# Kernel tuning notes

Measured on AMD Instinct MI355X. Metric: run time of the kernel, lower is better.

Reference implementation:

```python
import jax, jax.numpy as jnp
import numpy as np

H = 1024
E = 8
TOP_K = 2
B, S = 4, 2048


def setup_inputs() -> dict:
    key = jax.random.key(0)
    ks = jax.random.split(key, 8)
    scale = 0.02
    return {
        "x": jax.random.normal(ks[0], (B, S, H), dtype=jnp.float32),
        "router_w": jax.random.normal(ks[1], (H, E), dtype=jnp.float32) * scale,
        "router_b": jnp.zeros((E,), dtype=jnp.float32),
        "w1": jax.random.normal(ks[2], (E, H, 4 * H), dtype=jnp.float32) * scale,
        "b1": jnp.zeros((E, 4 * H), dtype=jnp.float32),
        "w2": jax.random.normal(ks[3], (E, 4 * H, H), dtype=jnp.float32) * scale,
        "b2": jnp.zeros((E, H), dtype=jnp.float32),
    }


def reference(x, router_w, router_b, w1, b1, w2, b2):
    b, s, h = x.shape
    n_exp = w1.shape[0]
    x_flat = x.reshape(-1, h)  # [T, H]
    T = x_flat.shape[0]

    # Router: softmax then top-k, renormalize top-k probs (matches torch code).
    logits = x_flat @ router_w + router_b            # [T, E]
    probs = jax.nn.softmax(logits, axis=-1)
    top_values, top_indices = jax.lax.top_k(probs, TOP_K)  # [T, k]
    top_values = top_values / jnp.sum(top_values, axis=-1, keepdims=True)

    # Per-token combine weight for each expert (0 if token not routed there).
    combine = jnp.zeros((T, n_exp), dtype=x.dtype)
    combine = combine.at[jnp.arange(T)[:, None], top_indices].add(top_values)  # [T, E]

    # Loop over the small fixed expert set; masked combine weights zero out
    # contributions from unrouted tokens, matching the gather/scatter original.
    out = jnp.zeros_like(x_flat)
    for e in range(n_exp):
        hmid = jax.nn.gelu(x_flat @ w1[e] + b1[e], approximate=False)  # [T, 4H]
        y = hmid @ w2[e] + b2[e]                                       # [T, H]
        out = out + combine[:, e:e + 1] * y
    return out.reshape(b, s, h)
```

## Files before the change

kernel.cpp:

```cpp
#include <hip/hip_runtime.h>
#include <hip/hip_bf16.h>
#include <math.h>

#define TT 8192
#define HD 1024
#define FHD 4096
#define NE 8
#define NTMAX 136
#define NWG1 4352

typedef short s16x8 __attribute__((ext_vector_type(8)));
typedef float f32x4 __attribute__((ext_vector_type(4)));
using bf16 = __hip_bfloat16;
typedef unsigned int u32;

#define OFF_COUNTS 0
#define OFF_DONE   32
#define OFF_CURSOR 64
#define OFF_OFFS   128
#define OFF_E0     256
#define OFF_E1     (OFF_E0 + 4*TT)
#define OFF_W0     (OFF_E1 + 4*TT)
#define OFF_W1     (OFF_W0 + 4*TT)
#define OFF_S0     (OFF_W1 + 4*TT)
#define OFF_S1     (OFF_S0 + 4*TT)
#define OFF_TID    (OFF_S1 + 4*TT)
#define OFF_TW     (OFF_TID + 8*TT)
#define OFF_TMR    (OFF_TW + 8*TT)
#define OFF_TME    (OFF_TMR + 4*144)
#define OFF_TMN    (OFF_TME + 4*144)
#define OFF_XBF    (OFF_TMN + 64)
#define OFF_W1T    (OFF_XBF + 2*TT*HD)
#define OFF_W2T    (OFF_W1T + 2*NE*HD*FHD)
#define OFF_HMID   (OFF_W2T + 2*NE*HD*FHD)
#define OFF_YS     (OFF_HMID + (size_t)2*(2*TT)*FHD)

__device__ __forceinline__ void gload_lds16(const void* g, void* l) {
    __builtin_amdgcn_global_load_lds(
        (const __attribute__((address_space(1))) u32*)g,
        (__attribute__((address_space(3))) u32*)l, 16, 0, 0);
}

__device__ __forceinline__ void transpose_panel(const float* __restrict__ in,
        bf16* __restrict__ out, int R, int C, int rem, int tid, char* smem) {
    float (*tile)[65]  = reinterpret_cast<float(*)[65]>(smem);
    bf16  (*btile)[264] = reinterpret_cast<bf16(*)[264]>(smem + 16640);
    int kch = R >> 8, nch = C >> 6;
    int per = kch * nch;
    int e = rem / per;
    int rem2 = rem % per;
    int kc = rem2 / nch, nc = rem2 % nch;
    int k0 = kc << 8, n0 = nc << 6;
    const float* ine = in + (size_t)e * R * C;
    bf16* oute = out + (size_t)e * R * C;
    for (int s = 0; s < 4; ++s) {
        int ks = k0 + s * 64;
#pragma unroll
        for (int i = 0; i < 4; ++i) {
            int lin = tid + i * 256;
            int r = lin >> 4, cg = lin & 15;
            float4 v = *reinterpret_cast<const float4*>(&ine[(size_t)(ks + r) * C + n0 + cg * 4]);
            tile[r][cg * 4 + 0] = v.x; tile[r][cg * 4 + 1] = v.y;
            tile[r][cg * 4 + 2] = v.z; tile[r][cg * 4 + 3] = v.w;
        }
        __syncthreads();
#pragma unroll
        for (int i = 0; i < 4; ++i) {
            int lin = tid + i * 256;
            int n = lin >> 4, kg = lin & 15;
            bf16 h[4];
            h[0] = __float2bfloat16(tile[kg * 4 + 0][n]);
            h[1] = __float2bfloat16(tile[kg * 4 + 1][n]);
            h[2] = __float2bfloat16(tile[kg * 4 + 2][n]);
            h[3] = __float2bfloat16(tile[kg * 4 + 3][n]);
            *reinterpret_cast<uint2*>(&btile[n][s * 64 + kg * 4]) = *reinterpret_cast<uint2*>(h);
        }
        __syncthreads();
    }
#pragma unroll
    for (int i = 0; i < 8; ++i) {
        int lin = tid + i * 256;
        int n = lin >> 5, kk = lin & 31;
        *reinterpret_cast<uint4*>(&oute[(size_t)(n0 + n) * R + k0 + kk * 8]) =
            *reinterpret_cast<const uint4*>(&btile[n][kk * 8]);
    }
}

__global__ __launch_bounds__(256) void fused1_kernel(
        const float* __restrict__ x, const float* __restrict__ rw, const float* __restrict__ rb,
        const float* __restrict__ w1, bf16* __restrict__ xbf, bf16* __restrict__ w1t,
        int* __restrict__ e0a, int* __restrict__ e1a,
        float* __restrict__ w0a, float* __restrict__ w1a,
        int* __restrict__ counts, int* __restrict__ done,
        int* __restrict__ offs, int* __restrict__ cursor,
        int* __restrict__ tmr, int* __restrict__ tme, int* __restrict__ tmn) {
    __shared__ __attribute__((aligned(16))) char smem[50432];
    int bid = blockIdx.x;
    int tid = threadIdx.x;
    if (bid < 2048) {
        transpose_panel(w1, w1t, HD, FHD, bid, tid, smem);
        return;
    }
    int rbid = bid - 2048;
    int wid = tid >> 6, lane = tid & 63;
    int t = rbid * 4 + wid;
    const float* xp = x + (size_t)t * HD + lane * 16;
    float xv[16];
#pragma unroll
    for (int j = 0; j < 4; ++j) {
        float4 v = *reinterpret_cast<const float4*>(&xp[j * 4]);
        xv[4 * j] = v.x; xv[4 * j + 1] = v.y; xv[4 * j + 2] = v.z; xv[4 * j + 3] = v.w;
    }
    {
        bf16 hv[16];
#pragma unroll
        for (int j = 0; j < 16; ++j) hv[j] = __float2bfloat16(xv[j]);
        uint4* dst = reinterpret_cast<uint4*>(&xbf[(size_t)t * HD + lane * 16]);
        dst[0] = reinterpret_cast<uint4*>(hv)[0];
        dst[1] = reinterpret_cast<uint4*>(hv)[1];
    }
    float acc[8] = {0.f, 0.f, 0.f, 0.f, 0.f, 0.f, 0.f, 0.f};
    const float* rp = rw + (size_t)(lane * 16) * NE;
#pragma unroll
    for (int hh = 0; hh < 16; ++hh) {
        float4 r0 = *reinterpret_cast<const float4*>(&rp[hh * 8]);
        float4 r1 = *reinterpret_cast<const float4*>(&rp[hh * 8 + 4]);
        acc[0] += xv[hh] * r0.x; acc[1] += xv[hh] * r0.y;
        acc[2] += xv[hh] * r0.z; acc[3] += xv[hh] * r0.w;
        acc[4] += xv[hh] * r1.x; acc[5] += xv[hh] * r1.y;
        acc[6] += xv[hh] * r1.z; acc[7] += xv[hh] * r1.w;
    }
#pragma unroll
    for (int e = 0; e < 8; ++e) {
#pragma unroll
        for (int off = 32; off > 0; off >>= 1) acc[e] += __shfl_xor(acc[e], off, 64);
    }
    if (lane == 0) {
        float lg[8];
#pragma unroll
        for (int e = 0; e < 8; ++e) lg[e] = acc[e] + rb[e];
        int a = 0;
#pragma unroll
        for (int e = 1; e < 8; ++e) if (lg[e] > lg[a]) a = e;
        int b = (a == 0) ? 1 : 0;
#pragma unroll
        for (int e = 0; e < 8; ++e) if (e != a && e != b && lg[e] > lg[b]) b = e;
        float wa = 1.0f / (1.0f + expf(lg[b] - lg[a]));
        float wb = 1.0f / (1.0f + expf(lg[a] - lg[b]));
        e0a[t] = a; e1a[t] = b; w0a[t] = wa; w1a[t] = wb;
        atomicAdd(&counts[a], 1);
        atomicAdd(&counts[b], 1);
    }
    __syncthreads();
    __shared__ int lastFlag;
    if (tid == 0) {
        __threadfence();
        lastFlag = (atomicAdd(done, 1) == 2047) ? 1 : 0;
    }
    __syncthreads();
    if (!lastFlag) return;
    __threadfence();
    __shared__ int cbase[NE + 1], tbase[NE + 1];
    if (tid == 0) {
        int s = 0, ntt = 0;
        for (int e = 0; e < NE; ++e) {
            int c = atomicAdd(&counts[e], 0);
            cbase[e] = s; tbase[e] = ntt;
            s += c; ntt += (c + 127) >> 7;
        }
        cbase[NE] = s; tbase[NE] = ntt;
        tmn[0] = ntt;
        offs[NE] = s;
    }
    __syncthreads();
    if (tid < NE) { offs[tid] = cbase[tid]; cursor[tid] = cbase[tid]; }
    if (tid < NTMAX) {
        int ntt = tbase[NE];
        if (tid < ntt) {
            int e = 0;
            while (tbase[e + 1] <= tid) ++e;
            tmr[tid] = cbase[e] + ((tid - tbase[e]) << 7);
            tme[tid] = e;
        } else { tmr[tid] = 0; tme[tid] = 0; }
    }
}

__global__ __launch_bounds__(256) void scatter_kernel(const int* __restrict__ e0a, const int* __restrict__ e1a,
        const float* __restrict__ w0a, const float* __restrict__ w1a,
        int* __restrict__ cursor, int* __restrict__ tid_arr, float* __restrict__ tw_arr,
        int* __restrict__ slot0, int* __restrict__ slot1) {
    int t = blockIdx.x * 256 + threadIdx.x;
    int s0 = atomicAdd(&cursor[e0a[t]], 1);
    tid_arr[s0] = t; tw_arr[s0] = w0a[t]; slot0[t] = s0;
    int s1 = atomicAdd(&cursor[e1a[t]], 1);
    tid_arr[s1] = t; tw_arr[s1] = w1a[t]; slot1[t] = s1;
}

__global__ __launch_bounds__(256) void fused2_kernel(
        const float* __restrict__ w2, bf16* __restrict__ w2t,
        const bf16* __restrict__ xbf, const bf16* __restrict__ w1t,
        const float* __restrict__ b1, const int* __restrict__ offs,
        const int* __restrict__ tid_arr, bf16* __restrict__ hmid,
        const int* __restrict__ tmr, const int* __restrict__ tme, const int* __restrict__ tmn) {
    __shared__ __attribute__((aligned(16))) char smem[50432];
    int bid = blockIdx.x;
    int tid = threadIdx.x;
    if (bid < 2048) {
        transpose_panel(w2, w2t, FHD, HD, bid, tid, smem);
        return;
    }
    bf16* As = reinterpret_cast<bf16*>(smem);
    bf16* Bs = reinterpret_cast<bf16*>(smem + 8192);
    int*  toks = reinterpret_cast<int*>(smem + 16384);
    int orig = bid - 2048;
    int wg = (orig & 7) * (NWG1 >> 3) + (orig >> 3);
    int st = wg / 68, within = wg % 68;
    int tidx = (st >> 3) * 17 + (within % 17);
    int nt = (st & 7) * 4 + (within / 17);
    if (tidx >= tmn[0]) return;
    int e = tme[tidx];
    int row0 = tmr[tidx];
    int s1 = offs[e + 1];
    int n0 = nt * 128;
    if (tid < 128) { int s = row0 + tid; toks[tid] = tid_arr[(s < s1) ? s : (s1 - 1)]; }
    __syncthreads();
    int lane = tid & 63, w = tid >> 6;
    int wrow = (w >> 1) * 64, wcol = (w & 1) * 64;
    int lr = lane & 15, lk = (lane >> 4) * 8;
    int srow = lane >> 2, seg = lane & 3;
    int tokA0 = toks[w * 32 + srow];
    int tokA1 = toks[w * 32 + 16 + srow];
    const bf16* w1e = w1t + (size_t)e * FHD * HD;
    const bf16* bsrc0 = w1e + (size_t)(n0 + w * 32 + srow) * HD + seg * 8;
    const bf16* bsrc1 = w1e + (size_t)(n0 + w * 32 + 16 + srow) * HD + seg * 8;
    const bf16* asrc0 = xbf + (size_t)tokA0 * HD + seg * 8;
    const bf16* asrc1 = xbf + (size_t)tokA1 * HD + seg * 8;
    bf16* aDst0 = &As[(w * 32) * 32];
    bf16* aDst1 = &As[(w * 32 + 16) * 32];
    bf16* bDst0 = &Bs[(w * 32) * 32];
    bf16* bDst1 = &Bs[(w * 32 + 16) * 32];
    f32x4 acc[4][4] = {};
    for (int k0 = 0; k0 < HD; k0 += 32) {
        gload_lds16(asrc0 + k0, aDst0);
        gload_lds16(asrc1 + k0, aDst1);
        gload_lds16(bsrc0 + k0, bDst0);
        gload_lds16(bsrc1 + k0, bDst1);
        __syncthreads();
        s16x8 aF[4], bF[4];
#pragma unroll
        for (int m = 0; m < 4; ++m) aF[m] = *reinterpret_cast<const s16x8*>(&As[(wrow + m * 16 + lr) * 32 + lk]);
#pragma unroll
        for (int n = 0; n < 4; ++n) bF[n] = *reinterpret_cast<const s16x8*>(&Bs[(wcol + n * 16 + lr) * 32 + lk]);
#pragma unroll
        for (int m = 0; m < 4; ++m)
#pragma unroll
            for (int n = 0; n < 4; ++n)
                acc[m][n] = __builtin_amdgcn_mfma_f32_16x16x32_bf16(aF[m], bF[n], acc[m][n], 0, 0, 0);
        __syncthreads();
    }
#pragma unroll
    for (int m = 0; m < 4; ++m) {
#pragma unroll
        for (int n = 0; n < 4; ++n) {
            int col = n0 + wcol + n * 16 + lr;
            float bv = b1[(size_t)e * FHD + col];
#pragma unroll
            for (int r = 0; r < 4; ++r) {
                int row = wrow + m * 16 + (lane >> 4) * 4 + r;
                int slot = row0 + row;
                if (slot < s1) {
                    float v2 = acc[m][n][r] + bv;
                    v2 = 0.5f * v2 * (1.0f + erff(v2 * 0.70710678118f));
                    hmid[(size_t)slot * FHD + col] = __float2bfloat16(v2);
                }
            }
        }
    }
}

__global__ __launch_bounds__(256) void gemm2_kernel(const bf16* __restrict__ hmid, const bf16* __restrict__ w2t,
        const float* __restrict__ b2, const int* __restrict__ offs, float* __restrict__ ys,
        const int* __restrict__ tmr, const int* __restrict__ tme, const int* __restrict__ tmn) {
    __shared__ bf16 As[128 * 32];
    __shared__ bf16 Bs[128 * 32];
    int nwg = gridDim.x;
    int orig = blockIdx.x;
    int wg = (orig & 7) * (nwg >> 3) + (orig >> 3);
    int st = wg / 34, within = wg % 34;
    int tidx = (st >> 2) * 17 + (within % 17);
    int nt = (st & 3) * 2 + (within / 17);
    if (tidx >= tmn[0]) return;
    int e = tme[tidx];
    int row0 = tmr[tidx];
    int s1 = offs[e + 1];
    int n0 = nt * 128;
    int tid = threadIdx.x;
    int lane = tid & 63, w = tid >> 6;
    int wrow = (w >> 1) * 64, wcol = (w & 1) * 64;
    int lr = lane & 15, lk = (lane >> 4) * 8;
    int srow = lane >> 2, seg = lane & 3;
    int ar0 = row0 + w * 32 + srow;      if (ar0 >= s1) ar0 = s1 - 1;
    int ar1 = row0 + w * 32 + 16 + srow; if (ar1 >= s1) ar1 = s1 - 1;
    const bf16* w2e = w2t + (size_t)e * HD * FHD;
    const bf16* bsrc0 = w2e + (size_t)(n0 + w * 32 + srow) * FHD + seg * 8;
    const bf16* bsrc1 = w2e + (size_t)(n0 + w * 32 + 16 + srow) * FHD + seg * 8;
    const bf16* asrc0 = hmid + (size_t)ar0 * FHD + seg * 8;
    const bf16* asrc1 = hmid + (size_t)ar1 * FHD + seg * 8;
    bf16* aDst0 = &As[(w * 32) * 32];
    bf16* aDst1 = &As[(w * 32 + 16) * 32];
    bf16* bDst0 = &Bs[(w * 32) * 32];
    bf16* bDst1 = &Bs[(w * 32 + 16) * 32];
    f32x4 acc[4][4] = {};
    for (int k0 = 0; k0 < FHD; k0 += 32) {
        gload_lds16(asrc0 + k0, aDst0);
        gload_lds16(asrc1 + k0, aDst1);
        gload_lds16(bsrc0 + k0, bDst0);
        gload_lds16(bsrc1 + k0, bDst1);
        __syncthreads();
        s16x8 aF[4], bF[4];
#pragma unroll
        for (int m = 0; m < 4; ++m) aF[m] = *reinterpret_cast<const s16x8*>(&As[(wrow + m * 16 + lr) * 32 + lk]);
#pragma unroll
        for (int n = 0; n < 4; ++n) bF[n] = *reinterpret_cast<const s16x8*>(&Bs[(wcol + n * 16 + lr) * 32 + lk]);
#pragma unroll
        for (int m = 0; m < 4; ++m)
#pragma unroll
            for (int n = 0; n < 4; ++n)
                acc[m][n] = __builtin_amdgcn_mfma_f32_16x16x32_bf16(aF[m], bF[n], acc[m][n], 0, 0, 0);
        __syncthreads();
    }
#pragma unroll
    for (int m = 0; m < 4; ++m) {
#pragma unroll
        for (int n = 0; n < 4; ++n) {
            int col = n0 + wcol + n * 16 + lr;
            float bv = b2[(size_t)e * HD + col];
#pragma unroll
            for (int r = 0; r < 4; ++r) {
                int row = wrow + m * 16 + (lane >> 4) * 4 + r;
                int slot = row0 + row;
                if (slot < s1) ys[(size_t)slot * HD + col] = acc[m][n][r] + bv;
            }
        }
    }
}

__global__ __launch_bounds__(256) void combine_kernel(const float* __restrict__ ys,
        const int* __restrict__ slot0, const int* __restrict__ slot1,
        const float* __restrict__ tw, float* __restrict__ out) {
    int t = blockIdx.x;
    int c = threadIdx.x * 4;
    int sa = slot0[t], sb = slot1[t];
    float wa = tw[sa], wb = tw[sb];
    float4 a = *reinterpret_cast<const float4*>(&ys[(size_t)sa * HD + c]);
    float4 b = *reinterpret_cast<const float4*>(&ys[(size_t)sb * HD + c]);
    float4 o;
    o.x = wa * a.x + wb * b.x; o.y = wa * a.y + wb * b.y;
    o.z = wa * a.z + wb * b.z; o.w = wa * a.w + wb * b.w;
    *reinterpret_cast<float4*>(&out[(size_t)t * HD + c]) = o;
}

extern "C" void kernel_launch(void* const* d_in, const int* in_sizes, int n_in,
                              void* d_out, int out_size, void* d_ws, size_t ws_size,
                              hipStream_t stream) {
    const float* x  = (const float*)d_in[0];
    const float* rw = (const float*)d_in[1];
    const float* rb = (const float*)d_in[2];
    const float* w1 = (const float*)d_in[3];
    const float* b1 = (const float*)d_in[4];
    const float* w2 = (const float*)d_in[5];
    const float* b2 = (const float*)d_in[6];
    float* out = (float*)d_out;
    char* ws = (char*)d_ws;

    int*   counts  = (int*)(ws + OFF_COUNTS);
    int*   done    = (int*)(ws + OFF_DONE);
    int*   cursor  = (int*)(ws + OFF_CURSOR);
    int*   offs    = (int*)(ws + OFF_OFFS);
    int*   e0a     = (int*)(ws + OFF_E0);
    int*   e1a     = (int*)(ws + OFF_E1);
    float* w0a     = (float*)(ws + OFF_W0);
    float* w1a     = (float*)(ws + OFF_W1);
    int*   slot0   = (int*)(ws + OFF_S0);
    int*   slot1   = (int*)(ws + OFF_S1);
    int*   tid_arr = (int*)(ws + OFF_TID);
    float* tw_arr  = (float*)(ws + OFF_TW);
    int*   tmr     = (int*)(ws + OFF_TMR);
    int*   tme     = (int*)(ws + OFF_TME);
    int*   tmn     = (int*)(ws + OFF_TMN);
    bf16*  xbf     = (bf16*)(ws + OFF_XBF);
    bf16*  w1t     = (bf16*)(ws + OFF_W1T);
    bf16*  w2t     = (bf16*)(ws + OFF_W2T);
    bf16*  hmid    = (bf16*)(ws + OFF_HMID);
    float* ys      = (float*)(ws + OFF_YS);

    hipMemsetAsync(counts, 0, 64, stream);

    fused1_kernel<<<4096, 256, 0, stream>>>(x, rw, rb, w1, xbf, w1t,
        e0a, e1a, w0a, w1a, counts, done, offs, cursor, tmr, tme, tmn);
    scatter_kernel<<<TT / 256, 256, 0, stream>>>(e0a, e1a, w0a, w1a, cursor,
        tid_arr, tw_arr, slot0, slot1);
    fused2_kernel<<<2048 + NWG1, 256, 0, stream>>>(w2, w2t, xbf, w1t, b1, offs,
        tid_arr, hmid, tmr, tme, tmn);
    gemm2_kernel<<<(HD / 128) * NTMAX, 256, 0, stream>>>(hmid, w2t, b2, offs, ys, tmr, tme, tmn);
    combine_kernel<<<TT, 256, 0, stream>>>(ys, slot0, slot1, tw_arr, out);
}
```

Before: 880.4 us.

## Double-buffer LDS tiles in both expert GEMM kernels to overlap loads with MFMA

Both the fused GEMM1+GELU kernel and the GEMM2 kernel now use two LDS buffers for the A and B tiles. Each iteration issues the global-to-LDS loads for the next K step before running the MFMAs on the current buffer. This drops the per-iteration barrier that used to separate loading from compute, so memory latency can hide behind matrix math. In exchange GEMM2 doubles its LDS footprint, which may lower occupancy. Correctness also depends on the existing end-of-loop barrier waiting for the async LDS loads to finish.

```diff
diff --git a/kernel.cpp b/kernel.cpp
--- a/kernel.cpp
+++ b/kernel.cpp
@@ -210,8 +210,8 @@
         return;
     }
     bf16* As = reinterpret_cast<bf16*>(smem);
-    bf16* Bs = reinterpret_cast<bf16*>(smem + 8192);
-    int*  toks = reinterpret_cast<int*>(smem + 16384);
+    bf16* Bs = reinterpret_cast<bf16*>(smem + 16384);
+    int*  toks = reinterpret_cast<int*>(smem + 32768);
     int orig = bid - 2048;
     int wg = (orig & 7) * (NWG1 >> 3) + (orig >> 3);
     int st = wg / 68, within = wg % 68;
@@ -235,22 +235,31 @@
     const bf16* bsrc1 = w1e + (size_t)(n0 + w * 32 + 16 + srow) * HD + seg * 8;
     const bf16* asrc0 = xbf + (size_t)tokA0 * HD + seg * 8;
     const bf16* asrc1 = xbf + (size_t)tokA1 * HD + seg * 8;
-    bf16* aDst0 = &As[(w * 32) * 32];
-    bf16* aDst1 = &As[(w * 32 + 16) * 32];
-    bf16* bDst0 = &Bs[(w * 32) * 32];
-    bf16* bDst1 = &Bs[(w * 32 + 16) * 32];
+    int d0 = (w * 32) * 32 + srow * 32 + seg * 8;
+    int d1 = (w * 32 + 16) * 32 + srow * 32 + seg * 8;
     f32x4 acc[4][4] = {};
-    for (int k0 = 0; k0 < HD; k0 += 32) {
-        gload_lds16(asrc0 + k0, aDst0);
-        gload_lds16(asrc1 + k0, aDst1);
-        gload_lds16(bsrc0 + k0, bDst0);
-        gload_lds16(bsrc1 + k0, bDst1);
-        __syncthreads();
+    gload_lds16(asrc0, &As[d0]);
+    gload_lds16(asrc1, &As[d1]);
+    gload_lds16(bsrc0, &Bs[d0]);
+    gload_lds16(bsrc1, &Bs[d1]);
+    __syncthreads();
+    const int NK = HD / 32;
+    for (int kt = 0; kt < NK; ++kt) {
+        int cur = kt & 1;
+        if (kt + 1 < NK) {
+            int nb = (cur ^ 1) * 4096, ko = (kt + 1) * 32;
+            gload_lds16(asrc0 + ko, &As[nb + d0]);
+            gload_lds16(asrc1 + ko, &As[nb + d1]);
+            gload_lds16(bsrc0 + ko, &Bs[nb + d0]);
+            gload_lds16(bsrc1 + ko, &Bs[nb + d1]);
+        }
+        const bf16* Ab = &As[cur * 4096];
+        const bf16* Bb = &Bs[cur * 4096];
         s16x8 aF[4], bF[4];
 #pragma unroll
-        for (int m = 0; m < 4; ++m) aF[m] = *reinterpret_cast<const s16x8*>(&As[(wrow + m * 16 + lr) * 32 + lk]);
-#pragma unroll
-        for (int n = 0; n < 4; ++n) bF[n] = *reinterpret_cast<const s16x8*>(&Bs[(wcol + n * 16 + lr) * 32 + lk]);
+        for (int m = 0; m < 4; ++m) aF[m] = *reinterpret_cast<const s16x8*>(&Ab[(wrow + m * 16 + lr) * 32 + lk]);
+#pragma unroll
+        for (int n = 0; n < 4; ++n) bF[n] = *reinterpret_cast<const s16x8*>(&Bb[(wcol + n * 16 + lr) * 32 + lk]);
 #pragma unroll
         for (int m = 0; m < 4; ++m)
 #pragma unroll
@@ -281,8 +290,8 @@
 __global__ __launch_bounds__(256) void gemm2_kernel(const bf16* __restrict__ hmid, const bf16* __restrict__ w2t,
         const float* __restrict__ b2, const int* __restrict__ offs, float* __restrict__ ys,
         const int* __restrict__ tmr, const int* __restrict__ tme, const int* __restrict__ tmn) {
-    __shared__ bf16 As[128 * 32];
-    __shared__ bf16 Bs[128 * 32];
+    __shared__ bf16 As[2][128 * 32];
+    __shared__ bf16 Bs[2][128 * 32];
     int nwg = gridDim.x;
     int orig = blockIdx.x;
     int wg = (orig & 7) * (nwg >> 3) + (orig >> 3);
@@ -306,22 +315,29 @@
     const bf16* bsrc1 = w2e + (size_t)(n0 + w * 32 + 16 + srow) * FHD + seg * 8;
     const bf16* asrc0 = hmid + (size_t)ar0 * FHD + seg * 8;
     const bf16* asrc1 = hmid + (size_t)ar1 * FHD + seg * 8;
-    bf16* aDst0 = &As[(w * 32) * 32];
-    bf16* aDst1 = &As[(w * 32 + 16) * 32];
-    bf16* bDst0 = &Bs[(w * 32) * 32];
-    bf16* bDst1 = &Bs[(w * 32 + 16) * 32];
+    int d0 = (w * 32) * 32 + srow * 32 + seg * 8;
+    int d1 = (w * 32 + 16) * 32 + srow * 32 + seg * 8;
     f32x4 acc[4][4] = {};
-    for (int k0 = 0; k0 < FHD; k0 += 32) {
-        gload_lds16(asrc0 + k0, aDst0);
-        gload_lds16(asrc1 + k0, aDst1);
-        gload_lds16(bsrc0 + k0, bDst0);
-        gload_lds16(bsrc1 + k0, bDst1);
-        __syncthreads();
+    gload_lds16(asrc0, &As[0][d0]);
+    gload_lds16(asrc1, &As[0][d1]);
+    gload_lds16(bsrc0, &Bs[0][d0]);
+    gload_lds16(bsrc1, &Bs[0][d1]);
+    __syncthreads();
+    const int NK = FHD / 32;
+    for (int kt = 0; kt < NK; ++kt) {
+        int cur = kt & 1;
+        if (kt + 1 < NK) {
+            int nb = cur ^ 1, ko = (kt + 1) * 32;
+            gload_lds16(asrc0 + ko, &As[nb][d0]);
+            gload_lds16(asrc1 + ko, &As[nb][d1]);
+            gload_lds16(bsrc0 + ko, &Bs[nb][d0]);
+            gload_lds16(bsrc1 + ko, &Bs[nb][d1]);
+        }
         s16x8 aF[4], bF[4];
 #pragma unroll
-        for (int m = 0; m < 4; ++m) aF[m] = *reinterpret_cast<const s16x8*>(&As[(wrow + m * 16 + lr) * 32 + lk]);
-#pragma unroll
-        for (int n = 0; n < 4; ++n) bF[n] = *reinterpret_cast<const s16x8*>(&Bs[(wcol + n * 16 + lr) * 32 + lk]);
+        for (int m = 0; m < 4; ++m) aF[m] = *reinterpret_cast<const s16x8*>(&As[cur][(wrow + m * 16 + lr) * 32 + lk]);
+#pragma unroll
+        for (int n = 0; n < 4; ++n) bF[n] = *reinterpret_cast<const s16x8*>(&Bs[cur][(wcol + n * 16 + lr) * 32 + lk]);
 #pragma unroll
         for (int m = 0; m < 4; ++m)
 #pragma unroll
```

New measurement: 898.7 us. 2.1% more time.
